# Kernel optimization log

Measured on AMD Instinct MI355X. Metric: run time of the kernel, lower is better.

## Reference

```python
import jax, jax.numpy as jnp
import numpy as np

B, S, N, D, QD = 32, 256, 50, 100, 768


def _xavier(key, fan_out, fan_in):
    lim = float(np.sqrt(6.0 / (fan_in + fan_out)))
    return jax.random.uniform(key, (fan_out, fan_in), jnp.float32, -lim, lim)


def setup_inputs() -> dict:
    key = jax.random.key(0)
    ks = jax.random.split(key, 8)
    q = jax.random.normal(ks[0], (B, QD), jnp.float32)
    k = jax.random.normal(ks[1], (B, S, N, D), jnp.float32)
    v = jax.random.normal(ks[2], (B, S, N, D), jnp.float32)
    input_ent = jax.random.randint(ks[3], (B, S), 0, 100000)
    Q_w = _xavier(ks[4], D, QD)
    V_w = _xavier(ks[5], D, D)
    bq = 1.0 / np.sqrt(QD)
    bv = 1.0 / np.sqrt(D)
    Q_b = jax.random.uniform(ks[6], (D,), jnp.float32, -bq, bq)
    V_b = jax.random.uniform(ks[7], (D,), jnp.float32, -bv, bv)
    return {"input_ent": input_ent, "q": q, "k": k, "v": v,
            "Q_w": Q_w, "Q_b": Q_b, "V_w": V_w, "V_b": V_b}


def reference(input_ent, q, k, v, Q_w, Q_b, V_w, V_b):
    # Q projection + L2 normalize over feature dim (F.normalize eps=1e-12)
    Q = q @ Q_w.T + Q_b                                            # [B, D]
    Qn = Q / jnp.maximum(jnp.linalg.norm(Q, axis=1, keepdims=True), 1e-12)
    # Keys/values share the same V_linear projection of v (k arg unused, as in source)
    K = jnp.einsum('bsnd,ed->bsne', v, V_w) + V_b                  # [B, S, N, D]
    # detached L2 norm with zero->1e-6 replacement
    l2 = jax.lax.stop_gradient(jnp.linalg.norm(K, axis=3, keepdims=True))
    l2 = jnp.where(l2 == 0.0, 1e-6, l2)
    Kn = K / l2
    # cosine-similarity scores over neighbors
    att = jnp.einsum('bd,bsnd->bsn', Qn, Kn)                       # [B, S, N]
    att = jnp.where(att == 0.0, -10000.0, att)
    att = jax.nn.softmax(jax.nn.leaky_relu(att, 0.01), axis=2)
    # zero out positions where softmax was exactly uniform (pad rows)
    att = jnp.where(att == 1.0 / att.shape[-1], 0.0, att)
    # weighted sum of values (V_linear(v) == K)
    out = jnp.einsum('bsn,bsnd->bsd', att, K)                      # [B, S, D]
    # mode == 'candidate': return combined directly (graphsage=False)
    return out
```

## Files before the change

### kernel.cpp

```cpp
#include <hip/hip_runtime.h>
#include <math.h>


#define S_DIM 256
#define N_NBR 50
#define D_F   100
#define QD    768
#define NT    7
#define KC    4
#define TILE_F4 1250
#define ITERS 16

typedef __attribute__((ext_vector_type(4))) float f32x4;
typedef __attribute__((ext_vector_type(8))) short s16x8;
typedef __attribute__((ext_vector_type(4))) short s16x4;

__device__ __forceinline__ short f2bf(float f) {
  union { float f; unsigned u; } x; x.f = f;
  unsigned r = x.u + 0x7fffu + ((x.u >> 16) & 1u);
  return (short)(r >> 16);
}

__global__ __launch_bounds__(256, 2) void wga_kernel(
    const float* __restrict__ v, const float* __restrict__ q,
    const float* __restrict__ Qw, const float* __restrict__ Qb,
    const float* __restrict__ Vw, const float* __restrict__ Vb,
    float* __restrict__ out) {
  __shared__ __align__(16) short Abuf[KC * 4 * 64 * 8];
  __shared__ float Kl[N_NBR + 2][105];
  __shared__ __align__(16) float attS[64];
  __shared__ float QnS[112];
  __shared__ float nrm2[64], srw[64];
  __shared__ float qs[QD];
  __shared__ float Qpart[256];
  __shared__ float rnS;

  const int t  = threadIdx.x;
  const int w  = t >> 6, l = t & 63;
  const int qd = l >> 4, m = l & 15;
  const int blk = blockIdx.x;
  const int b   = blk >> 4;
  const int s0  = (blk & 15) * ITERS;

  f32x4 pf[5];
  {
    const f32x4* vt = (const f32x4*)(v + (size_t)(b * S_DIM + s0) * (N_NBR * D_F));
#pragma unroll
    for (int j = 0; j < 5; ++j) {
      const int i = t + 256 * j;
      if (i < TILE_F4) pf[j] = vt[i];
    }
  }

  s16x8 bfrag[NT][KC];
  float bias[NT], QnSv[NT];
#pragma unroll
  for (int nt = 0; nt < NT; ++nt) {
    const int e = nt * 16 + m;
    bias[nt] = (e < D_F) ? Vb[e] : 0.f;
#pragma unroll
    for (int c = 0; c < KC; ++c) {
      const int k0 = c * 32 + qd * 8;
      s16x8 pk;
#pragma unroll
      for (int j = 0; j < 8; ++j) {
        const int k = k0 + j;
        const float x = (e < D_F && k < D_F) ? Vw[e * D_F + k] : 0.f;
        pk[j] = f2bf(x);
      }
      bfrag[nt][c] = pk;
    }
  }

  {
    int4* az = (int4*)Abuf;
    for (int i = t; i < 1024; i += 256) az[i] = make_int4(0, 0, 0, 0);
    float* klz = &Kl[N_NBR][0];
    if (t < 210) klz[t] = 0.f;
    for (int i = t; i < QD; i += 256) qs[i] = q[b * QD + i];
  }
  __syncthreads();

  if (t < 200) {
    const int e = t >> 1, h = t & 1;
    const float4* wr = (const float4*)(Qw + e * QD + h * 384);
    const float4* qv = (const float4*)(qs + h * 384);
    float a0 = 0.f, a1 = 0.f, a2 = 0.f, a3 = 0.f;
#pragma unroll 4
    for (int f = 0; f < 96; ++f) {
      float4 wv = wr[f], qf = qv[f];
      a0 += wv.x * qf.x; a1 += wv.y * qf.y; a2 += wv.z * qf.z; a3 += wv.w * qf.w;
    }
    Qpart[t] = (a0 + a1) + (a2 + a3);
  }
  __syncthreads();
  if (t < D_F)       QnS[t] = Qpart[2 * t] + Qpart[2 * t + 1] + Qb[t];
  else if (t < 112)  QnS[t] = 0.f;
  __syncthreads();
  if (w == 0) {
    float x = QnS[l] * QnS[l];
    if (l < 48) x += QnS[64 + l] * QnS[64 + l];
#pragma unroll
    for (int d = 1; d < 64; d <<= 1) x += __shfl_xor(x, d, 64);
    if (l == 0) rnS = 1.0f / fmaxf(sqrtf(x), 1e-12f);
  }
  __syncthreads();
  if (t < D_F) QnS[t] *= rnS;
  __syncthreads();
#pragma unroll
  for (int nt = 0; nt < NT; ++nt) QnSv[nt] = QnS[nt * 16 + m];

  for (int it = 0; it < ITERS; ++it) {
#pragma unroll
    for (int j = 0; j < 5; ++j) {
      const int i = t + 256 * j;
      if (i < TILE_F4) {
        const int n  = i / 25;
        const int k4 = (i - n * 25) * 4;
        const int wv = n >> 4, mm = n & 15;
        const int c = k4 >> 5, qq = (k4 >> 3) & 3, j0 = k4 & 7;
        s16x4 p;
        p[0] = f2bf(pf[j][0]); p[1] = f2bf(pf[j][1]);
        p[2] = f2bf(pf[j][2]); p[3] = f2bf(pf[j][3]);
        *(s16x4*)&Abuf[(((c * 4 + wv) * 64 + qq * 16 + mm) << 3) + j0] = p;
      }
    }
    __syncthreads();

    if (it + 1 < ITERS) {
      const f32x4* vt = (const f32x4*)(v + (size_t)(b * S_DIM + s0 + it + 1) * (N_NBR * D_F));
#pragma unroll
      for (int j = 0; j < 5; ++j) {
        const int i = t + 256 * j;
        if (i < TILE_F4) pf[j] = vt[i];
      }
    }

    f32x4 acc[NT];
#pragma unroll
    for (int nt = 0; nt < NT; ++nt) {
      f32x4 z; z[0] = bias[nt]; z[1] = bias[nt]; z[2] = bias[nt]; z[3] = bias[nt];
      acc[nt] = z;
    }
    s16x8 af[KC];
#pragma unroll
    for (int c = 0; c < KC; ++c)
      af[c] = *(const s16x8*)&Abuf[((c * 4 + w) * 64 + l) * 8];
#pragma unroll
    for (int c = 0; c < KC; ++c)
#pragma unroll
      for (int nt = 0; nt < NT; ++nt)
        acc[nt] = __builtin_amdgcn_mfma_f32_16x16x32_bf16(af[c], bfrag[nt][c], acc[nt], 0, 0, 0);

#pragma unroll
    for (int r = 0; r < 4; ++r) {
      float np = 0.f, sp = 0.f;
#pragma unroll
      for (int nt = 0; nt < NT; ++nt) {
        const float kv = acc[nt][r];
        np += kv * kv;
        sp += QnSv[nt] * kv;
      }
#pragma unroll
      for (int d = 1; d < 16; d <<= 1) {
        np += __shfl_xor(np, d, 64);
        sp += __shfl_xor(sp, d, 64);
      }
      if (m == 0) {
        const int row = w * 16 + qd * 4 + r;
        nrm2[row] = np; srw[row] = sp;
      }
    }
#pragma unroll
    for (int nt = 0; nt < NT; ++nt) {
      const int col = nt * 16 + m;
#pragma unroll
      for (int r = 0; r < 4; ++r) {
        const int row = w * 16 + qd * 4 + r;
        if (row < N_NBR && col < D_F) Kl[row][col] = acc[nt][r];
      }
    }
    __syncthreads();

    if (w == 0) {
      float a = -1e30f;
      if (l < N_NBR) {
        float l2 = sqrtf(nrm2[l]);
        if (l2 == 0.f) l2 = 1e-6f;
        float sc = srw[l] / l2;
        if (sc == 0.f) sc = -10000.f;
        a = (sc >= 0.f) ? sc : 0.01f * sc;
      }
      float mx = a;
#pragma unroll
      for (int d = 1; d < 64; d <<= 1) mx = fmaxf(mx, __shfl_xor(mx, d, 64));
      const float e = (l < N_NBR) ? __expf(a - mx) : 0.f;
      float sm = e;
#pragma unroll
      for (int d = 1; d < 64; d <<= 1) sm += __shfl_xor(sm, d, 64);
      float att = e / sm;
      if (att == 0.02f) att = 0.f;
      attS[l] = (l < N_NBR) ? att : 0.f;
    }
    __syncthreads();

    if (t < D_F) {
      float o = 0.f;
#pragma unroll
      for (int c = 0; c < 13; ++c) {
        float4 av = *(const float4*)&attS[c * 4];
        o += av.x * Kl[c * 4 + 0][t];
        o += av.y * Kl[c * 4 + 1][t];
        o += av.z * Kl[c * 4 + 2][t];
        o += av.w * Kl[c * 4 + 3][t];
      }
      out[(size_t)(b * S_DIM + s0 + it) * D_F + t] = o;
    }
  }
}

extern "C" void kernel_launch(void* const* d_in, const int* in_sizes, int n_in,
                              void* d_out, int out_size, void* d_ws, size_t ws_size,
                              hipStream_t stream) {
  const float* q  = (const float*)d_in[1];
  const float* v  = (const float*)d_in[3];
  const float* Qw = (const float*)d_in[4];
  const float* Qb = (const float*)d_in[5];
  const float* Vw = (const float*)d_in[6];
  const float* Vb = (const float*)d_in[7];
  float* out = (float*)d_out;
  (void)d_ws; (void)ws_size;

  wga_kernel<<<512, 256, 0, stream>>>(v, q, Qw, Qb, Vw, Vb, out);
}
```

Baseline: 345.1 us.

## Quadruple grid size, swizzle A buffer, and alias prologue LDS with Kl

After: 414.8 us. +20.2%, slower.

```diff
diff --git a/kernel.cpp b/kernel.cpp
--- a/kernel.cpp
+++ b/kernel.cpp
@@ -9,7 +9,8 @@
 #define NT    7
 #define KC    4
 #define TILE_F4 1250
-#define ITERS 16
+#define ITERS 4
+#define KLS   108
 
 typedef __attribute__((ext_vector_type(4))) float f32x4;
 typedef __attribute__((ext_vector_type(8))) short s16x8;
@@ -19,6 +20,10 @@
   union { float f; unsigned u; } x; x.f = f;
   unsigned r = x.u + 0x7fffu + ((x.u >> 16) & 1u);
   return (short)(r >> 16);
+}
+
+__device__ __forceinline__ int agran(int c, int wv, int qq, int mm) {
+  return ((c * 4 + wv) << 6) + (qq << 4) + (mm ^ (qq << 1));
 }
 
 __global__ __launch_bounds__(256, 2) void wga_kernel(
@@ -27,20 +32,21 @@
     const float* __restrict__ Vw, const float* __restrict__ Vb,
     float* __restrict__ out) {
   __shared__ __align__(16) short Abuf[KC * 4 * 64 * 8];
-  __shared__ float Kl[N_NBR + 2][105];
+  __shared__ union {
+    float Kl[N_NBR + 2][KLS];
+    struct { float qs[QD]; float Qpart[256]; } pre;
+  } U;
   __shared__ __align__(16) float attS[64];
   __shared__ float QnS[112];
   __shared__ float nrm2[64], srw[64];
-  __shared__ float qs[QD];
-  __shared__ float Qpart[256];
   __shared__ float rnS;
 
   const int t  = threadIdx.x;
   const int w  = t >> 6, l = t & 63;
   const int qd = l >> 4, m = l & 15;
   const int blk = blockIdx.x;
-  const int b   = blk >> 4;
-  const int s0  = (blk & 15) * ITERS;
+  const int b   = blk >> 6;
+  const int s0  = (blk & 63) * ITERS;
 
   f32x4 pf[5];
   {
@@ -50,6 +56,12 @@
       const int i = t + 256 * j;
       if (i < TILE_F4) pf[j] = vt[i];
     }
+  }
+
+  {
+    int4* az = (int4*)Abuf;
+    for (int i = t; i < 1024; i += 256) az[i] = make_int4(0, 0, 0, 0);
+    for (int i = t; i < QD; i += 256) U.pre.qs[i] = q[b * QD + i];
   }
 
   s16x8 bfrag[NT][KC];
@@ -71,30 +83,22 @@
       bfrag[nt][c] = pk;
     }
   }
-
-  {
-    int4* az = (int4*)Abuf;
-    for (int i = t; i < 1024; i += 256) az[i] = make_int4(0, 0, 0, 0);
-    float* klz = &Kl[N_NBR][0];
-    if (t < 210) klz[t] = 0.f;
-    for (int i = t; i < QD; i += 256) qs[i] = q[b * QD + i];
-  }
   __syncthreads();
 
   if (t < 200) {
     const int e = t >> 1, h = t & 1;
     const float4* wr = (const float4*)(Qw + e * QD + h * 384);
-    const float4* qv = (const float4*)(qs + h * 384);
+    const float4* qv = (const float4*)(U.pre.qs + h * 384);
     float a0 = 0.f, a1 = 0.f, a2 = 0.f, a3 = 0.f;
 #pragma unroll 4
     for (int f = 0; f < 96; ++f) {
       float4 wv = wr[f], qf = qv[f];
       a0 += wv.x * qf.x; a1 += wv.y * qf.y; a2 += wv.z * qf.z; a3 += wv.w * qf.w;
     }
-    Qpart[t] = (a0 + a1) + (a2 + a3);
-  }
-  __syncthreads();
-  if (t < D_F)       QnS[t] = Qpart[2 * t] + Qpart[2 * t + 1] + Qb[t];
+    U.pre.Qpart[t] = (a0 + a1) + (a2 + a3);
+  }
+  __syncthreads();
+  if (t < D_F)       QnS[t] = U.pre.Qpart[2 * t] + U.pre.Qpart[2 * t + 1] + Qb[t];
   else if (t < 112)  QnS[t] = 0.f;
   __syncthreads();
   if (w == 0) {
@@ -103,6 +107,10 @@
 #pragma unroll
     for (int d = 1; d < 64; d <<= 1) x += __shfl_xor(x, d, 64);
     if (l == 0) rnS = 1.0f / fmaxf(sqrtf(x), 1e-12f);
+  }
+  {
+    float* klz = &U.Kl[N_NBR][0];
+    if (t < 2 * KLS) klz[t] = 0.f;
   }
   __syncthreads();
   if (t < D_F) QnS[t] *= rnS;
@@ -122,7 +130,7 @@
         s16x4 p;
         p[0] = f2bf(pf[j][0]); p[1] = f2bf(pf[j][1]);
         p[2] = f2bf(pf[j][2]); p[3] = f2bf(pf[j][3]);
-        *(s16x4*)&Abuf[(((c * 4 + wv) * 64 + qq * 16 + mm) << 3) + j0] = p;
+        *(s16x4*)&Abuf[(agran(c, wv, qq, mm) << 3) + j0] = p;
       }
     }
     __syncthreads();
@@ -145,7 +153,7 @@
     s16x8 af[KC];
 #pragma unroll
     for (int c = 0; c < KC; ++c)
-      af[c] = *(const s16x8*)&Abuf[((c * 4 + w) * 64 + l) * 8];
+      af[c] = *(const s16x8*)&Abuf[agran(c, w, l >> 4, l & 15) << 3];
 #pragma unroll
     for (int c = 0; c < KC; ++c)
 #pragma unroll
@@ -177,7 +185,7 @@
 #pragma unroll
       for (int r = 0; r < 4; ++r) {
         const int row = w * 16 + qd * 4 + r;
-        if (row < N_NBR && col < D_F) Kl[row][col] = acc[nt][r];
+        if (row < N_NBR && col < D_F) U.Kl[row][col] = acc[nt][r];
       }
     }
     __syncthreads();
@@ -209,10 +217,10 @@
 #pragma unroll
       for (int c = 0; c < 13; ++c) {
         float4 av = *(const float4*)&attS[c * 4];
-        o += av.x * Kl[c * 4 + 0][t];
-        o += av.y * Kl[c * 4 + 1][t];
-        o += av.z * Kl[c * 4 + 2][t];
-        o += av.w * Kl[c * 4 + 3][t];
+        o += av.x * U.Kl[c * 4 + 0][t];
+        o += av.y * U.Kl[c * 4 + 1][t];
+        o += av.z * U.Kl[c * 4 + 2][t];
+        o += av.w * U.Kl[c * 4 + 3][t];
       }
       out[(size_t)(b * S_DIM + s0 + it) * D_F + t] = o;
     }
@@ -231,5 +239,5 @@
   float* out = (float*)d_out;
   (void)d_ws; (void)ws_size;
 
-  wga_kernel<<<512, 256, 0, stream>>>(v, q, Qw, Qb, Vw, Vb, out);
-}
+  wga_kernel<<<2048, 256, 0, stream>>>(v, q, Qw, Qb, Vw, Vb, out);
+}
```
